# Kernel optimization log

Hardware: AMD Instinct MI355X
Metric: run time of the kernel (lower is better)

The kernel has to match this reference:

```python
import jax, jax.numpy as jnp
import numpy as np

EPS = 1e-5
NUM_MEM_TOKENS = 16
SEGMENT_SIZE = 512


def dpfp(x):
    # DPFP feature map (Schlag et al.), nu=1: doubles the last dim, all-nonnegative.
    x2 = jnp.concatenate([jax.nn.relu(x), jax.nn.relu(-x)], axis=-1)
    return x2 * jnp.roll(x2, 1, axis=-1)


def setup_inputs() -> dict:
    key = jax.random.key(0)
    ks = jax.random.split(key, 7)
    B, S, D, DM = 4, 4224, 1024, 64  # S = n_seg * (segment_size + num_mem_tokens) = 8*528
    scale = 0.02
    return {
        "hidden_states": jax.random.normal(ks[0], (B, S, D), jnp.float32),
        "model_output": jax.random.normal(ks[1], (B, S, D), jnp.float32),
        "W_mq": jax.random.normal(ks[2], (D, DM), jnp.float32) * scale,
        "W_mk": jax.random.normal(ks[3], (D, DM), jnp.float32) * scale,
        "W_mv": jax.random.normal(ks[4], (D, D), jnp.float32) * scale,
        "W_mb": jax.random.normal(ks[5], (D, D), jnp.float32) * scale,
        "b_mb": jnp.zeros((D,), jnp.float32),
    }


def reference(hidden_states, model_output, W_mq, W_mk, W_mv, W_mb, b_mb):
    B, S, D = hidden_states.shape
    L = SEGMENT_SIZE + NUM_MEM_TOKENS
    n_seg = S // L
    d_key = 2 * W_mq.shape[1]  # dpfp doubles feature dim

    # [n_seg, B, L, D]
    h = hidden_states.reshape(B, n_seg, L, D).transpose(1, 0, 2, 3)
    m = model_output.reshape(B, n_seg, L, D).transpose(1, 0, 2, 3)

    def step(carry, seg):
        W_mem, z = carry  # [B, d_key, D], [B, d_key]
        hid, mo = seg     # [B, L, D] each
        # --- associate: linear-attention read of compressive memory ---
        q = dpfp(hid @ W_mq)                                   # [B, L, d_key]
        num = jnp.einsum('blk,bkd->bld', q, W_mem)             # [B, L, D]
        den = jnp.einsum('blk,bk->bl', q, z)[..., None] + EPS
        assoc = num / den
        # --- delta-rule memory update from memory tokens of segment output ---
        mem = (assoc + mo)[:, -NUM_MEM_TOKENS:]                # [B, M, D]
        k = dpfp(mem @ W_mk)                                   # [B, M, d_key]
        v = mem @ W_mv                                         # [B, M, D]
        gate = jax.nn.sigmoid(mem @ W_mb + b_mb)               # [B, M, D]
        prev = jnp.einsum('bmk,bkd->bmd', k, W_mem) / (
            jnp.einsum('bmk,bk->bm', k, z)[..., None] + EPS)   # correction (old value)
        new_info = gate * (v - prev)
        W_mem = W_mem + jnp.einsum('bmk,bmd->bkd', k, new_info)
        z = z + k.sum(axis=1)
        return (W_mem, z), assoc

    W0 = jnp.zeros((B, d_key, D), hidden_states.dtype)
    z0 = jnp.zeros((B, d_key), hidden_states.dtype)
    _, assocs = jax.lax.scan(step, (W0, z0), (h, m))           # [n_seg, B, L, D]
    association = jnp.tanh(assocs.transpose(1, 0, 2, 3).reshape(B, S, D))
    return model_output + association
```

## Files before the change

kernel.cpp:

```cpp
#include <hip/hip_runtime.h>
#include <hip/hip_bf16.h>

#define EPS 1e-5f

typedef short s8v __attribute__((ext_vector_type(8)));
typedef short s4v __attribute__((ext_vector_type(4)));
typedef float f4v __attribute__((ext_vector_type(4)));

__device__ __forceinline__ unsigned short f2bf(float f) {
  unsigned u = __builtin_bit_cast(unsigned, f);
  u = u + 0x7FFFu + ((u >> 16) & 1u);
  return (unsigned short)(u >> 16);
}
__device__ __forceinline__ float bf2f(unsigned short h) {
  unsigned u = ((unsigned)h) << 16;
  return __builtin_bit_cast(float, u);
}
__device__ __forceinline__ float fast_tanh(float x) {
  float e = __expf(2.0f * x);
  return 1.0f - 2.0f / (e + 1.0f);
}
__device__ __forceinline__ float fast_sigmoid(float x) {
  return 1.0f / (1.0f + __expf(-x));
}

__global__ __launch_bounds__(256) void transpose_kernel(
    const float* __restrict__ W_mq, const float* __restrict__ W_mk,
    const float* __restrict__ W_mv, const float* __restrict__ W_mb,
    unsigned short* __restrict__ W_mqT, unsigned short* __restrict__ W_mkT,
    unsigned short* __restrict__ W_mvT, unsigned short* __restrict__ W_mbT) {
  __shared__ float tile[32][33];
  int bid = blockIdx.x;
  const float* src; unsigned short* dst; int N, t0;
  if (bid < 64)        { src = W_mq; dst = W_mqT; N = 64;   t0 = bid; }
  else if (bid < 128)  { src = W_mk; dst = W_mkT; N = 64;   t0 = bid - 64; }
  else if (bid < 1152) { src = W_mv; dst = W_mvT; N = 1024; t0 = bid - 128; }
  else                 { src = W_mb; dst = W_mbT; N = 1024; t0 = bid - 1152; }
  const int K = 1024;
  int tk = t0 & 31, tn = t0 >> 5;
  int k0 = tk * 32, n0 = tn * 32;
  int t = threadIdx.x;
  int cr = t >> 5, cc = t & 31;
#pragma unroll
  for (int u = 0; u < 4; u++) {
    int row = cr + u * 8;
    tile[row][cc] = src[(size_t)(k0 + row) * N + n0 + cc];
  }
  __syncthreads();
#pragma unroll
  for (int u = 0; u < 4; u++) {
    int nl = cr + u * 8;
    dst[(size_t)(n0 + nl) * K + k0 + cc] = f2bf(tile[cc][nl]);
  }
}

__global__ __launch_bounds__(128) void q_kernel(
    const float* __restrict__ HS, const unsigned short* __restrict__ W_mqT,
    unsigned short* __restrict__ Q) {
  __shared__ __align__(16) union { float y[16 * 64]; unsigned short kq[16 * 128]; } lds;
  int t = threadIdx.x, wv = t >> 6, lane = t & 63, m = lane & 15, q = lane >> 4;
  int r0 = blockIdx.x * 16;
  const float* ap = HS + (size_t)(r0 + m) * 1024 + wv * 512 + q * 8;
  const unsigned short* bp = W_mqT + (size_t)m * 1024 + wv * 512 + q * 8;
  f4v acc[4] = {f4v{0,0,0,0}, f4v{0,0,0,0}, f4v{0,0,0,0}, f4v{0,0,0,0}};
#pragma unroll 4
  for (int ks = 0; ks < 16; ks++) {
    int k0 = ks * 32;
    f4v h0 = *(const f4v*)(ap + k0);
    f4v h1 = *(const f4v*)(ap + k0 + 4);
    s8v a;
    a[0] = (short)f2bf(h0[0]); a[1] = (short)f2bf(h0[1]);
    a[2] = (short)f2bf(h0[2]); a[3] = (short)f2bf(h0[3]);
    a[4] = (short)f2bf(h1[0]); a[5] = (short)f2bf(h1[1]);
    a[6] = (short)f2bf(h1[2]); a[7] = (short)f2bf(h1[3]);
#pragma unroll
    for (int nf = 0; nf < 4; nf++) {
      s8v b = *(const s8v*)(bp + nf * 16384 + k0);
      acc[nf] = __builtin_amdgcn_mfma_f32_16x16x32_bf16(a, b, acc[nf], 0, 0, 0);
    }
  }
  if (wv == 1) {
#pragma unroll
    for (int nf = 0; nf < 4; nf++)
#pragma unroll
      for (int i = 0; i < 4; i++)
        lds.y[(nf * 4 + i) * 64 + lane] = acc[nf][i];
  }
  __syncthreads();
  if (wv == 0) {
#pragma unroll
    for (int nf = 0; nf < 4; nf++)
#pragma unroll
      for (int i = 0; i < 4; i++)
        acc[nf][i] += lds.y[(nf * 4 + i) * 64 + lane];
    int srcl = (lane & 48) | ((m + 15) & 15);
#pragma unroll
    for (int i = 0; i < 4; i++) {
      float yp[4];
#pragma unroll
      for (int nf = 0; nf < 4; nf++) yp[nf] = __shfl(acc[nf][i], srcl);
      int r = q * 4 + i;
#pragma unroll
      for (int nf = 0; nf < 4; nf++) {
        float yv = acc[nf][i];
        float py = (m != 0) ? yp[nf] : (nf > 0 ? yp[nf - 1] : yp[3]);
        bool wrap = (m == 0 && nf == 0);
        float x2lo = wrap ? fmaxf(-py, 0.f) : fmaxf(py, 0.f);
        float x2hi = wrap ? fmaxf(py, 0.f) : fmaxf(-py, 0.f);
        lds.kq[r * 128 + nf * 16 + m]      = f2bf(fmaxf(yv, 0.f) * x2lo);
        lds.kq[r * 128 + 64 + nf * 16 + m] = f2bf(fmaxf(-yv, 0.f) * x2hi);
      }
    }
  }
  __syncthreads();
  {
    int row = t >> 3, ch = t & 7;
    unsigned short* qp = Q + (size_t)(r0 + row) * 128 + ch * 16;
    *(s8v*)(qp)     = *(const s8v*)&lds.kq[row * 128 + ch * 16];
    *(s8v*)(qp + 8) = *(const s8v*)&lds.kq[row * 128 + ch * 16 + 8];
  }
}

__device__ __forceinline__ void assoc_tile(
    const unsigned short* __restrict__ Qb, const unsigned short* __restrict__ WmemT_s,
    const float* __restrict__ z_s, const float* __restrict__ MO,
    float* __restrict__ OUT, unsigned short* __restrict__ mem_bf,
    int seg, int rt, int ct, int b, bool write_mem) {
  int lane = threadIdx.x & 63, m = lane & 15, q = lane >> 4;
  size_t grow = (size_t)b * 4224 + seg * 528 + rt * 16;
  const unsigned short* qp = Qb + (grow + m) * 128;
  const float* zp = z_s + b * 128 + q * 8;
  s8v a[4];
  float dp = 0.f;
#pragma unroll
  for (int ks = 0; ks < 4; ks++) {
    a[ks] = *(const s8v*)(qp + ks * 32 + q * 8);
    f4v z0 = *(const f4v*)(zp + ks * 32);
    f4v z1 = *(const f4v*)(zp + ks * 32 + 4);
#pragma unroll
    for (int j = 0; j < 4; j++) dp += bf2f((unsigned short)a[ks][j]) * z0[j];
#pragma unroll
    for (int j = 0; j < 4; j++) dp += bf2f((unsigned short)a[ks][j + 4]) * z1[j];
  }
  dp += __shfl_xor(dp, 16);
  dp += __shfl_xor(dp, 32);
  dp += EPS;
  f4v acc[4] = {f4v{0,0,0,0}, f4v{0,0,0,0}, f4v{0,0,0,0}, f4v{0,0,0,0}};
  const unsigned short* wp = WmemT_s + ((size_t)b * 1024 + ct * 64 + m) * 128;
#pragma unroll
  for (int ks = 0; ks < 4; ks++) {
#pragma unroll
    for (int nf = 0; nf < 4; nf++) {
      s8v bv = *(const s8v*)(wp + nf * 2048 + ks * 32 + q * 8);
      acc[nf] = __builtin_amdgcn_mfma_f32_16x16x32_bf16(a[ks], bv, acc[nf], 0, 0, 0);
    }
  }
#pragma unroll
  for (int i = 0; i < 4; i++) {
    float den = __shfl(dp, q * 4 + i);
    int lrow = rt * 16 + q * 4 + i;
    size_t rbase = ((size_t)b * 4224 + seg * 528 + lrow) * 1024;
#pragma unroll
    for (int nf = 0; nf < 4; nf++) {
      int col = ct * 64 + nf * 16 + m;
      float assoc = acc[nf][i] / den;
      float mov = MO[rbase + col];
      OUT[rbase + col] = mov + fast_tanh(assoc);
      if (write_mem)
        mem_bf[(size_t)(b * 16 + (lrow - 512)) * 1024 + col] = f2bf(assoc + mov);
    }
  }
}

__global__ __launch_bounds__(64) void a_mem_kernel(
    const unsigned short* __restrict__ Qb, const unsigned short* __restrict__ WmemT_s,
    const float* __restrict__ z_s, const float* __restrict__ MO,
    float* __restrict__ OUT, unsigned short* __restrict__ mem_bf, int seg) {
  assoc_tile(Qb, WmemT_s, z_s, MO, OUT, mem_bf, seg, 32, blockIdx.x, blockIdx.y, true);
}

__global__ __launch_bounds__(64) void a_bulk_kernel(
    const unsigned short* __restrict__ Qb, const unsigned short* __restrict__ hist,
    const float* __restrict__ zh, const float* __restrict__ MO,
    float* __restrict__ OUT) {
  int seg = blockIdx.z >> 2, b = blockIdx.z & 3;
  assoc_tile(Qb, hist + (size_t)seg * 524288, zh + seg * 512, MO, OUT, nullptr,
             seg, blockIdx.x, blockIdx.y, b, false);
}

__global__ __launch_bounds__(256) void update_kernel(
    const unsigned short* __restrict__ mem_bf, const unsigned short* __restrict__ W_mkT,
    const unsigned short* __restrict__ W_mvT, const unsigned short* __restrict__ W_mbT,
    const float* __restrict__ z_s, const unsigned short* __restrict__ WmemT_s,
    const float* __restrict__ b_mb, float* __restrict__ W_mem,
    unsigned short* __restrict__ WmemT_next, float* __restrict__ z_next) {
  int ct = blockIdx.x, b = blockIdx.y;
  __shared__ float y_lds[16 * 64];
  __shared__ __align__(16) float k_f[16 * 128];
  __shared__ __align__(16) unsigned short k_bf[16 * 128];
  __shared__ float part[256];
  __shared__ float kden_l[16];
  __shared__ float ni_lds[16 * 65];
  int t = threadIdx.x, wv = t >> 6, lane = t & 63, m = lane & 15, q = lane >> 4;
  const unsigned short* ap = mem_bf + (size_t)(b * 16 + m) * 1024;
  {
    const unsigned short* bp = W_mkT + (size_t)(wv * 16 + m) * 1024;
    f4v acy = {0, 0, 0, 0};
    for (int ks = 0; ks < 32; ks++) {
      s8v av = *(const s8v*)(ap + ks * 32 + q * 8);
      s8v bv = *(const s8v*)(bp + ks * 32 + q * 8);
      acy = __builtin_amdgcn_mfma_f32_16x16x32_bf16(av, bv, acy, 0, 0, 0);
    }
#pragma unroll
    for (int i = 0; i < 4; i++) y_lds[(q * 4 + i) * 64 + wv * 16 + m] = acy[i];
  }
  __syncthreads();
  {
    int r = t >> 4, jg = t & 15;
    const float* yr = &y_lds[r * 64];
    const float* zz = z_s + b * 128;
    float pd = 0.f;
#pragma unroll
    for (int u = 0; u < 8; u++) {
      int jj = jg * 8 + u, jm = (jj + 127) & 127;
      float yj = (jj < 64) ? yr[jj] : -yr[jj - 64];
      float ym = (jm < 64) ? yr[jm] : -yr[jm - 64];
      float kv = fmaxf(yj, 0.f) * fmaxf(ym, 0.f);
      k_f[r * 128 + jj] = kv;
      k_bf[r * 128 + jj] = f2bf(kv);
      pd += kv * zz[jj];
    }
    part[t] = pd;
  }
  __syncthreads();
  if (t < 16) {
    float s = 0.f;
#pragma unroll
    for (int jg = 0; jg < 16; jg++) s += part[t * 16 + jg];
    kden_l[t] = s + EPS;
  }
  __syncthreads();
  int c = ct * 64 + wv * 16 + m;
  f4v accv = {0,0,0,0}, accg = {0,0,0,0}, accp = {0,0,0,0};
  {
    const unsigned short* bvp = W_mvT + (size_t)c * 1024;
    const unsigned short* bgp = W_mbT + (size_t)c * 1024;
    for (int ks = 0; ks < 32; ks++) {
      s8v av = *(const s8v*)(ap + ks * 32 + q * 8);
      s8v bv = *(const s8v*)(bvp + ks * 32 + q * 8);
      s8v bg = *(const s8v*)(bgp + ks * 32 + q * 8);
      accv = __builtin_amdgcn_mfma_f32_16x16x32_bf16(av, bv, accv, 0, 0, 0);
      accg = __builtin_amdgcn_mfma_f32_16x16x32_bf16(av, bg, accg, 0, 0, 0);
    }
    const unsigned short* bmp = WmemT_s + ((size_t)b * 1024 + c) * 128;
#pragma unroll
    for (int ks = 0; ks < 4; ks++) {
      s8v ak = *(const s8v*)&k_bf[m * 128 + ks * 32 + q * 8];
      s8v bm = *(const s8v*)(bmp + ks * 32 + q * 8);
      accp = __builtin_amdgcn_mfma_f32_16x16x32_bf16(ak, bm, accp, 0, 0, 0);
    }
  }
  float bmb = b_mb[c];
#pragma unroll
  for (int i = 0; i < 4; i++) {
    int r = q * 4 + i;
    float prev = accp[i] / kden_l[r];
    float g = fast_sigmoid(accg[i] + bmb);
    ni_lds[r * 65 + wv * 16 + m] = g * (accv[i] - prev);
  }
  __syncthreads();
  int cl = t & 63, kg = t >> 6, cc = ct * 64 + cl;
  float niv[16];
#pragma unroll
  for (int mm = 0; mm < 16; mm++) niv[mm] = ni_lds[mm * 65 + cl];
  float delta[32];
#pragma unroll
  for (int jj = 0; jj < 32; jj++) delta[jj] = 0.f;
#pragma unroll
  for (int mm = 0; mm < 16; mm++) {
    const float* kb = &k_f[mm * 128 + kg * 32];
    float nv = niv[mm];
#pragma unroll
    for (int ch = 0; ch < 8; ch++) {
      f4v kv4 = *(const f4v*)(kb + ch * 4);
#pragma unroll
      for (int jj = 0; jj < 4; jj++) delta[ch * 4 + jj] += kv4[jj] * nv;
    }
  }
  float* wmp = W_mem + (size_t)b * 131072 + cc;
  unsigned short* wtp = WmemT_next + ((size_t)b * 1024 + cc) * 128 + kg * 32;
#pragma unroll
  for (int c8 = 0; c8 < 4; c8++) {
    s8v pk;
#pragma unroll
    for (int u = 0; u < 8; u++) {
      int kk = kg * 32 + c8 * 8 + u;
      float nv = wmp[(size_t)kk * 1024] + delta[c8 * 8 + u];
      wmp[(size_t)kk * 1024] = nv;
      pk[u] = (short)f2bf(nv);
    }
    *(s8v*)(wtp + c8 * 8) = pk;
  }
  if (ct == 0 && t < 128) {
    float s = 0.f;
#pragma unroll
    for (int r = 0; r < 16; r++) s += k_f[r * 128 + t];
    z_next[b * 128 + t] = z_s[b * 128 + t] + s;
  }
}

extern "C" void kernel_launch(void* const* d_in, const int* in_sizes, int n_in,
                              void* d_out, int out_size, void* d_ws, size_t ws_size,
                              hipStream_t stream) {
  const float* HS  = (const float*)d_in[0];
  const float* MO  = (const float*)d_in[1];
  const float* W_mq = (const float*)d_in[2];
  const float* W_mk = (const float*)d_in[3];
  const float* W_mv = (const float*)d_in[4];
  const float* W_mb = (const float*)d_in[5];
  const float* b_mb = (const float*)d_in[6];
  float* OUT = (float*)d_out;

  char* wsb = (char*)d_ws;
  float*          W_mem  = (float*)(wsb + 0);
  unsigned short* hist   = (unsigned short*)(wsb + 2097152);
  float*          zh     = (float*)(wsb + 11534336);
  unsigned short* Qb     = (unsigned short*)(wsb + 11552768);
  unsigned short* W_mqT  = (unsigned short*)(wsb + 15878144);
  unsigned short* W_mkT  = (unsigned short*)(wsb + 16009216);
  unsigned short* W_mvT  = (unsigned short*)(wsb + 16140288);
  unsigned short* W_mbT  = (unsigned short*)(wsb + 18237440);
  unsigned short* mem_bf = (unsigned short*)(wsb + 20334592);

  (void)hipMemsetAsync(wsb, 0, 3145728, stream);
  (void)hipMemsetAsync(wsb + 11534336, 0, 2048, stream);
  transpose_kernel<<<2176, 256, 0, stream>>>(W_mq, W_mk, W_mv, W_mb,
                                             W_mqT, W_mkT, W_mvT, W_mbT);
  q_kernel<<<1056, 128, 0, stream>>>(HS, W_mqT, Qb);
  for (int s = 0; s < 8; s++) {
    const unsigned short* hs = hist + (size_t)s * 524288;
    unsigned short* hn = hist + (size_t)(s + 1) * 524288;
    const float* zs = zh + s * 512;
    float* zn = zh + (s + 1) * 512;
    a_mem_kernel<<<dim3(16, 4), 64, 0, stream>>>(Qb, hs, zs, MO, OUT, mem_bf, s);
    update_kernel<<<dim3(16, 4), 256, 0, stream>>>(mem_bf, W_mkT, W_mvT, W_mbT,
                                                   zs, hs, b_mb, W_mem, hn, zn);
  }
  a_bulk_kernel<<<dim3(32, 16, 32), 64, 0, stream>>>(Qb, hist, zh, MO, OUT);
}
```

Before: 491.2 us.

## Fuse segment scan into one persistent kernel with grid barriers and LDS-resident memory

Replaces the 16 per-segment launches (assoc-of-memory-tokens plus update) with a single persistent 64-block scan kernel. Each block keeps its W_mem slice in fp32 and bf16 in shared memory, and blocks synchronise between the associate and update phases through an atomic-counter grid barrier. The bulk association kernel is also reworked to 256-thread blocks that stage results in LDS and write coalesced float4 outputs. The aim is to remove launch overhead and global W_mem round-trips. The cost is reliance on spin barriers, which assume all 64 blocks are co-resident, and low parallelism during the scan.

```diff
diff --git a/kernel.cpp b/kernel.cpp
--- a/kernel.cpp
+++ b/kernel.cpp
@@ -2,6 +2,7 @@
 #include <hip/hip_bf16.h>
 
 #define EPS 1e-5f
+#define NBLK 64
 
 typedef short s8v __attribute__((ext_vector_type(8)));
 typedef short s4v __attribute__((ext_vector_type(4)));
@@ -23,6 +24,7 @@
 __device__ __forceinline__ float fast_sigmoid(float x) {
   return 1.0f / (1.0f + __expf(-x));
 }
+__device__ __forceinline__ float frcp(float x) { return __builtin_amdgcn_rcpf(x); }
 
 __global__ __launch_bounds__(256) void transpose_kernel(
     const float* __restrict__ W_mq, const float* __restrict__ W_mk,
@@ -121,191 +123,254 @@
   }
 }
 
-__device__ __forceinline__ void assoc_tile(
-    const unsigned short* __restrict__ Qb, const unsigned short* __restrict__ WmemT_s,
-    const float* __restrict__ z_s, const float* __restrict__ MO,
-    float* __restrict__ OUT, unsigned short* __restrict__ mem_bf,
-    int seg, int rt, int ct, int b, bool write_mem) {
-  int lane = threadIdx.x & 63, m = lane & 15, q = lane >> 4;
-  size_t grow = (size_t)b * 4224 + seg * 528 + rt * 16;
-  const unsigned short* qp = Qb + (grow + m) * 128;
-  const float* zp = z_s + b * 128 + q * 8;
-  s8v a[4];
-  float dp = 0.f;
-#pragma unroll
-  for (int ks = 0; ks < 4; ks++) {
-    a[ks] = *(const s8v*)(qp + ks * 32 + q * 8);
-    f4v z0 = *(const f4v*)(zp + ks * 32);
-    f4v z1 = *(const f4v*)(zp + ks * 32 + 4);
-#pragma unroll
-    for (int j = 0; j < 4; j++) dp += bf2f((unsigned short)a[ks][j]) * z0[j];
-#pragma unroll
-    for (int j = 0; j < 4; j++) dp += bf2f((unsigned short)a[ks][j + 4]) * z1[j];
-  }
-  dp += __shfl_xor(dp, 16);
-  dp += __shfl_xor(dp, 32);
-  dp += EPS;
-  f4v acc[4] = {f4v{0,0,0,0}, f4v{0,0,0,0}, f4v{0,0,0,0}, f4v{0,0,0,0}};
-  const unsigned short* wp = WmemT_s + ((size_t)b * 1024 + ct * 64 + m) * 128;
-#pragma unroll
-  for (int ks = 0; ks < 4; ks++) {
-#pragma unroll
-    for (int nf = 0; nf < 4; nf++) {
-      s8v bv = *(const s8v*)(wp + nf * 2048 + ks * 32 + q * 8);
-      acc[nf] = __builtin_amdgcn_mfma_f32_16x16x32_bf16(a[ks], bv, acc[nf], 0, 0, 0);
-    }
-  }
-#pragma unroll
-  for (int i = 0; i < 4; i++) {
-    float den = __shfl(dp, q * 4 + i);
-    int lrow = rt * 16 + q * 4 + i;
-    size_t rbase = ((size_t)b * 4224 + seg * 528 + lrow) * 1024;
-#pragma unroll
-    for (int nf = 0; nf < 4; nf++) {
-      int col = ct * 64 + nf * 16 + m;
-      float assoc = acc[nf][i] / den;
-      float mov = MO[rbase + col];
-      OUT[rbase + col] = mov + fast_tanh(assoc);
-      if (write_mem)
-        mem_bf[(size_t)(b * 16 + (lrow - 512)) * 1024 + col] = f2bf(assoc + mov);
-    }
-  }
-}
-
-__global__ __launch_bounds__(64) void a_mem_kernel(
-    const unsigned short* __restrict__ Qb, const unsigned short* __restrict__ WmemT_s,
-    const float* __restrict__ z_s, const float* __restrict__ MO,
-    float* __restrict__ OUT, unsigned short* __restrict__ mem_bf, int seg) {
-  assoc_tile(Qb, WmemT_s, z_s, MO, OUT, mem_bf, seg, 32, blockIdx.x, blockIdx.y, true);
-}
-
-__global__ __launch_bounds__(64) void a_bulk_kernel(
-    const unsigned short* __restrict__ Qb, const unsigned short* __restrict__ hist,
-    const float* __restrict__ zh, const float* __restrict__ MO,
-    float* __restrict__ OUT) {
-  int seg = blockIdx.z >> 2, b = blockIdx.z & 3;
-  assoc_tile(Qb, hist + (size_t)seg * 524288, zh + seg * 512, MO, OUT, nullptr,
-             seg, blockIdx.x, blockIdx.y, b, false);
-}
-
-__global__ __launch_bounds__(256) void update_kernel(
-    const unsigned short* __restrict__ mem_bf, const unsigned short* __restrict__ W_mkT,
+__global__ __launch_bounds__(256, 1) void scan_kernel(
+    const unsigned short* __restrict__ Qb, const unsigned short* __restrict__ W_mkT,
     const unsigned short* __restrict__ W_mvT, const unsigned short* __restrict__ W_mbT,
-    const float* __restrict__ z_s, const unsigned short* __restrict__ WmemT_s,
-    const float* __restrict__ b_mb, float* __restrict__ W_mem,
-    unsigned short* __restrict__ WmemT_next, float* __restrict__ z_next) {
-  int ct = blockIdx.x, b = blockIdx.y;
+    const float* __restrict__ b_mb, const float* __restrict__ MO,
+    float* __restrict__ OUT, unsigned short* __restrict__ hist,
+    float* __restrict__ zh, unsigned short* __restrict__ mem_bf, int* bar) {
+  __shared__ float Wf[128 * 64];
+  __shared__ __align__(16) unsigned short Wbf[64 * 132];
+  __shared__ __align__(16) unsigned short mem_l[16 * 1032];
   __shared__ float y_lds[16 * 64];
   __shared__ __align__(16) float k_f[16 * 128];
   __shared__ __align__(16) unsigned short k_bf[16 * 128];
   __shared__ float part[256];
   __shared__ float kden_l[16];
   __shared__ float ni_lds[16 * 65];
+  __shared__ float z_l[128];
+
   int t = threadIdx.x, wv = t >> 6, lane = t & 63, m = lane & 15, q = lane >> 4;
-  const unsigned short* ap = mem_bf + (size_t)(b * 16 + m) * 1024;
-  {
-    const unsigned short* bp = W_mkT + (size_t)(wv * 16 + m) * 1024;
-    f4v acy = {0, 0, 0, 0};
-    for (int ks = 0; ks < 32; ks++) {
-      s8v av = *(const s8v*)(ap + ks * 32 + q * 8);
-      s8v bv = *(const s8v*)(bp + ks * 32 + q * 8);
-      acy = __builtin_amdgcn_mfma_f32_16x16x32_bf16(av, bv, acy, 0, 0, 0);
-    }
-#pragma unroll
-    for (int i = 0; i < 4; i++) y_lds[(q * 4 + i) * 64 + wv * 16 + m] = acy[i];
+  int ct = blockIdx.x & 15, b = blockIdx.x >> 4;
+
+  for (int i = t; i < 128 * 64; i += 256) Wf[i] = 0.f;
+  for (int i = t; i < 64 * 132; i += 256) Wbf[i] = 0;
+  if (t < 128) z_l[t] = 0.f;
+  __syncthreads();
+
+  for (int s = 0; s < 8; s++) {
+    {
+      int col = t >> 2, koff = (t & 3) * 32;
+      const unsigned short* srcp = &Wbf[col * 132 + koff];
+      unsigned short* dstp = hist + (size_t)s * 524288 +
+                             ((size_t)b * 1024 + ct * 64 + col) * 128 + koff;
+#pragma unroll
+      for (int u = 0; u < 4; u++) *(s8v*)(dstp + u * 8) = *(const s8v*)(srcp + u * 8);
+      if (ct == 0 && t < 128) zh[s * 512 + b * 128 + t] = z_l[t];
+    }
+    {
+      size_t grow = (size_t)b * 4224 + s * 528 + 512;
+      const unsigned short* qp = Qb + (grow + m) * 128;
+      s8v a[4];
+      float dp = 0.f;
+#pragma unroll
+      for (int ks = 0; ks < 4; ks++) {
+        a[ks] = *(const s8v*)(qp + ks * 32 + q * 8);
+#pragma unroll
+        for (int j = 0; j < 8; j++)
+          dp += bf2f((unsigned short)a[ks][j]) * z_l[ks * 32 + q * 8 + j];
+      }
+      dp += __shfl_xor(dp, 16);
+      dp += __shfl_xor(dp, 32);
+      dp += EPS;
+      f4v acc = {0, 0, 0, 0};
+#pragma unroll
+      for (int ks = 0; ks < 4; ks++) {
+        s8v bv = *(const s8v*)&Wbf[(wv * 16 + m) * 132 + ks * 32 + q * 8];
+        acc = __builtin_amdgcn_mfma_f32_16x16x32_bf16(a[ks], bv, acc, 0, 0, 0);
+      }
+      unsigned short* mb = mem_bf + (s & 1) * 65536;
+#pragma unroll
+      for (int i = 0; i < 4; i++) {
+        float rden = frcp(__shfl(dp, q * 4 + i));
+        int col = ct * 64 + wv * 16 + m;
+        size_t rbase = (grow + q * 4 + i) * 1024;
+        float assoc = acc[i] * rden;
+        float mov = MO[rbase + col];
+        OUT[rbase + col] = mov + fast_tanh(assoc);
+        mb[(size_t)(b * 16 + q * 4 + i) * 1024 + col] = f2bf(assoc + mov);
+      }
+    }
+    __syncthreads();
+    if (t == 0) {
+      __threadfence();
+      atomicAdd(bar + s, 1);
+      while (atomicAdd(bar + s, 0) < NBLK) __builtin_amdgcn_s_sleep(2);
+      __threadfence();
+    }
+    __syncthreads();
+    {
+      const unsigned short* srcp = mem_bf + (s & 1) * 65536 + b * 16384;
+      int r = t >> 4, c0 = (t & 15) * 64;
+#pragma unroll
+      for (int u = 0; u < 8; u++)
+        *(s8v*)&mem_l[r * 1032 + c0 + u * 8] = *(const s8v*)(srcp + r * 1024 + c0 + u * 8);
+    }
+    __syncthreads();
+    {
+      const unsigned short* ap2 = &mem_l[m * 1032];
+      const unsigned short* bp = W_mkT + (size_t)(wv * 16 + m) * 1024;
+      f4v acy = {0, 0, 0, 0};
+      for (int ks = 0; ks < 32; ks++) {
+        s8v av = *(const s8v*)(ap2 + ks * 32 + q * 8);
+        s8v bv = *(const s8v*)(bp + ks * 32 + q * 8);
+        acy = __builtin_amdgcn_mfma_f32_16x16x32_bf16(av, bv, acy, 0, 0, 0);
+      }
+#pragma unroll
+      for (int i = 0; i < 4; i++) y_lds[(q * 4 + i) * 64 + wv * 16 + m] = acy[i];
+    }
+    __syncthreads();
+    {
+      int r = t >> 4, jg = t & 15;
+      const float* yr = &y_lds[r * 64];
+      float pd = 0.f;
+#pragma unroll
+      for (int u = 0; u < 8; u++) {
+        int jj = jg * 8 + u, jm = (jj + 127) & 127;
+        float yj = (jj < 64) ? yr[jj] : -yr[jj - 64];
+        float ym = (jm < 64) ? yr[jm] : -yr[jm - 64];
+        float kv = fmaxf(yj, 0.f) * fmaxf(ym, 0.f);
+        k_f[r * 128 + jj] = kv;
+        k_bf[r * 128 + jj] = f2bf(kv);
+        pd += kv * z_l[jj];
+      }
+      part[t] = pd;
+    }
+    __syncthreads();
+    if (t < 16) {
+      float ssum = 0.f;
+#pragma unroll
+      for (int jg = 0; jg < 16; jg++) ssum += part[t * 16 + jg];
+      kden_l[t] = ssum + EPS;
+    }
+    __syncthreads();
+    {
+      int c = ct * 64 + wv * 16 + m;
+      const unsigned short* ap2 = &mem_l[m * 1032];
+      const unsigned short* bvp = W_mvT + (size_t)c * 1024;
+      const unsigned short* bgp = W_mbT + (size_t)c * 1024;
+      f4v accv = {0,0,0,0}, accg = {0,0,0,0}, accp = {0,0,0,0};
+      for (int ks = 0; ks < 32; ks++) {
+        s8v av = *(const s8v*)(ap2 + ks * 32 + q * 8);
+        s8v bv = *(const s8v*)(bvp + ks * 32 + q * 8);
+        s8v bg = *(const s8v*)(bgp + ks * 32 + q * 8);
+        accv = __builtin_amdgcn_mfma_f32_16x16x32_bf16(av, bv, accv, 0, 0, 0);
+        accg = __builtin_amdgcn_mfma_f32_16x16x32_bf16(av, bg, accg, 0, 0, 0);
+      }
+#pragma unroll
+      for (int ks = 0; ks < 4; ks++) {
+        s8v ak = *(const s8v*)&k_bf[m * 128 + ks * 32 + q * 8];
+        s8v bm = *(const s8v*)&Wbf[(wv * 16 + m) * 132 + ks * 32 + q * 8];
+        accp = __builtin_amdgcn_mfma_f32_16x16x32_bf16(ak, bm, accp, 0, 0, 0);
+      }
+      float bmb = b_mb[c];
+#pragma unroll
+      for (int i = 0; i < 4; i++) {
+        int r = q * 4 + i;
+        float prev = accp[i] * frcp(kden_l[r]);
+        float g = fast_sigmoid(accg[i] + bmb);
+        ni_lds[r * 65 + wv * 16 + m] = g * (accv[i] - prev);
+      }
+    }
+    __syncthreads();
+    {
+      int cl = t & 63, kg = t >> 6;
+      float niv[16];
+#pragma unroll
+      for (int mm = 0; mm < 16; mm++) niv[mm] = ni_lds[mm * 65 + cl];
+      float delta[32];
+#pragma unroll
+      for (int jj = 0; jj < 32; jj++) delta[jj] = 0.f;
+#pragma unroll
+      for (int mm = 0; mm < 16; mm++) {
+        const float* kb = &k_f[mm * 128 + kg * 32];
+        float nv = niv[mm];
+#pragma unroll
+        for (int ch = 0; ch < 8; ch++) {
+          f4v kv4 = *(const f4v*)(kb + ch * 4);
+#pragma unroll
+          for (int jj = 0; jj < 4; jj++) delta[ch * 4 + jj] += kv4[jj] * nv;
+        }
+      }
+#pragma unroll
+      for (int c8 = 0; c8 < 4; c8++) {
+        s8v pk;
+#pragma unroll
+        for (int u = 0; u < 8; u++) {
+          int kk = kg * 32 + c8 * 8 + u;
+          float nv = Wf[kk * 64 + cl] + delta[c8 * 8 + u];
+          Wf[kk * 64 + cl] = nv;
+          pk[u] = (short)f2bf(nv);
+        }
+        *(s8v*)&Wbf[cl * 132 + kg * 32 + c8 * 8] = pk;
+      }
+      if (t < 128) {
+        float ssum = 0.f;
+#pragma unroll
+        for (int r = 0; r < 16; r++) ssum += k_f[r * 128 + t];
+        z_l[t] += ssum;
+      }
+    }
+    __syncthreads();
+  }
+}
+
+__global__ __launch_bounds__(256) void a_bulk_kernel(
+    const unsigned short* __restrict__ Qb, const unsigned short* __restrict__ hist,
+    const float* __restrict__ zh, const float* __restrict__ MO,
+    float* __restrict__ OUT) {
+  __shared__ float as_l[64 * 65];
+  int t = threadIdx.x, wv = t >> 6, lane = t & 63, m = lane & 15, q = lane >> 4;
+  int rt4 = blockIdx.x, ct = blockIdx.y;
+  int seg = blockIdx.z >> 2, b = blockIdx.z & 3;
+  const unsigned short* Wm = hist + (size_t)seg * 524288 + ((size_t)b * 1024 + ct * 64) * 128;
+  const float* zp = zh + seg * 512 + b * 128;
+  size_t grow = (size_t)b * 4224 + seg * 528 + rt4 * 64 + wv * 16;
+  const unsigned short* qp = Qb + (grow + m) * 128;
+  s8v a[4];
+  float dp = 0.f;
+#pragma unroll
+  for (int ks = 0; ks < 4; ks++) {
+    a[ks] = *(const s8v*)(qp + ks * 32 + q * 8);
+    f4v z0 = *(const f4v*)(zp + ks * 32 + q * 8);
+    f4v z1 = *(const f4v*)(zp + ks * 32 + q * 8 + 4);
+#pragma unroll
+    for (int j = 0; j < 4; j++) dp += bf2f((unsigned short)a[ks][j]) * z0[j];
+#pragma unroll
+    for (int j = 0; j < 4; j++) dp += bf2f((unsigned short)a[ks][j + 4]) * z1[j];
+  }
+  dp += __shfl_xor(dp, 16);
+  dp += __shfl_xor(dp, 32);
+  dp += EPS;
+  f4v acc[4] = {f4v{0,0,0,0}, f4v{0,0,0,0}, f4v{0,0,0,0}, f4v{0,0,0,0}};
+#pragma unroll
+  for (int ks = 0; ks < 4; ks++) {
+#pragma unroll
+    for (int nf = 0; nf < 4; nf++) {
+      s8v bv = *(const s8v*)(Wm + (size_t)(nf * 16 + m) * 128 + ks * 32 + q * 8);
+      acc[nf] = __builtin_amdgcn_mfma_f32_16x16x32_bf16(a[ks], bv, acc[nf], 0, 0, 0);
+    }
+  }
+#pragma unroll
+  for (int i = 0; i < 4; i++) {
+    float rden = frcp(__shfl(dp, q * 4 + i));
+#pragma unroll
+    for (int nf = 0; nf < 4; nf++)
+      as_l[(wv * 16 + q * 4 + i) * 65 + nf * 16 + m] = acc[nf][i] * rden;
   }
   __syncthreads();
   {
-    int r = t >> 4, jg = t & 15;
-    const float* yr = &y_lds[r * 64];
-    const float* zz = z_s + b * 128;
-    float pd = 0.f;
-#pragma unroll
-    for (int u = 0; u < 8; u++) {
-      int jj = jg * 8 + u, jm = (jj + 127) & 127;
-      float yj = (jj < 64) ? yr[jj] : -yr[jj - 64];
-      float ym = (jm < 64) ? yr[jm] : -yr[jm - 64];
-      float kv = fmaxf(yj, 0.f) * fmaxf(ym, 0.f);
-      k_f[r * 128 + jj] = kv;
-      k_bf[r * 128 + jj] = f2bf(kv);
-      pd += kv * zz[jj];
-    }
-    part[t] = pd;
-  }
-  __syncthreads();
-  if (t < 16) {
-    float s = 0.f;
-#pragma unroll
-    for (int jg = 0; jg < 16; jg++) s += part[t * 16 + jg];
-    kden_l[t] = s + EPS;
-  }
-  __syncthreads();
-  int c = ct * 64 + wv * 16 + m;
-  f4v accv = {0,0,0,0}, accg = {0,0,0,0}, accp = {0,0,0,0};
-  {
-    const unsigned short* bvp = W_mvT + (size_t)c * 1024;
-    const unsigned short* bgp = W_mbT + (size_t)c * 1024;
-    for (int ks = 0; ks < 32; ks++) {
-      s8v av = *(const s8v*)(ap + ks * 32 + q * 8);
-      s8v bv = *(const s8v*)(bvp + ks * 32 + q * 8);
-      s8v bg = *(const s8v*)(bgp + ks * 32 + q * 8);
-      accv = __builtin_amdgcn_mfma_f32_16x16x32_bf16(av, bv, accv, 0, 0, 0);
-      accg = __builtin_amdgcn_mfma_f32_16x16x32_bf16(av, bg, accg, 0, 0, 0);
-    }
-    const unsigned short* bmp = WmemT_s + ((size_t)b * 1024 + c) * 128;
-#pragma unroll
-    for (int ks = 0; ks < 4; ks++) {
-      s8v ak = *(const s8v*)&k_bf[m * 128 + ks * 32 + q * 8];
-      s8v bm = *(const s8v*)(bmp + ks * 32 + q * 8);
-      accp = __builtin_amdgcn_mfma_f32_16x16x32_bf16(ak, bm, accp, 0, 0, 0);
-    }
-  }
-  float bmb = b_mb[c];
-#pragma unroll
-  for (int i = 0; i < 4; i++) {
-    int r = q * 4 + i;
-    float prev = accp[i] / kden_l[r];
-    float g = fast_sigmoid(accg[i] + bmb);
-    ni_lds[r * 65 + wv * 16 + m] = g * (accv[i] - prev);
-  }
-  __syncthreads();
-  int cl = t & 63, kg = t >> 6, cc = ct * 64 + cl;
-  float niv[16];
-#pragma unroll
-  for (int mm = 0; mm < 16; mm++) niv[mm] = ni_lds[mm * 65 + cl];
-  float delta[32];
-#pragma unroll
-  for (int jj = 0; jj < 32; jj++) delta[jj] = 0.f;
-#pragma unroll
-  for (int mm = 0; mm < 16; mm++) {
-    const float* kb = &k_f[mm * 128 + kg * 32];
-    float nv = niv[mm];
-#pragma unroll
-    for (int ch = 0; ch < 8; ch++) {
-      f4v kv4 = *(const f4v*)(kb + ch * 4);
-#pragma unroll
-      for (int jj = 0; jj < 4; jj++) delta[ch * 4 + jj] += kv4[jj] * nv;
-    }
-  }
-  float* wmp = W_mem + (size_t)b * 131072 + cc;
-  unsigned short* wtp = WmemT_next + ((size_t)b * 1024 + cc) * 128 + kg * 32;
-#pragma unroll
-  for (int c8 = 0; c8 < 4; c8++) {
-    s8v pk;
-#pragma unroll
-    for (int u = 0; u < 8; u++) {
-      int kk = kg * 32 + c8 * 8 + u;
-      float nv = wmp[(size_t)kk * 1024] + delta[c8 * 8 + u];
-      wmp[(size_t)kk * 1024] = nv;
-      pk[u] = (short)f2bf(nv);
-    }
-    *(s8v*)(wtp + c8 * 8) = pk;
-  }
-  if (ct == 0 && t < 128) {
-    float s = 0.f;
-#pragma unroll
-    for (int r = 0; r < 16; r++) s += k_f[r * 128 + t];
-    z_next[b * 128 + t] = z_s[b * 128 + t] + s;
+    int r = t >> 2, cchunk = (t & 3) * 16;
+    size_t rbase = ((size_t)b * 4224 + seg * 528 + rt4 * 64 + r) * 1024 + ct * 64 + cchunk;
+    const float* ar = &as_l[r * 65 + cchunk];
+#pragma unroll
+    for (int u = 0; u < 4; u++) {
+      f4v mo = *(const f4v*)(MO + rbase + u * 4);
+      f4v o;
+#pragma unroll
+      for (int j = 0; j < 4; j++) o[j] = mo[j] + fast_tanh(ar[u * 4 + j]);
+      *(f4v*)(OUT + rbase + u * 4) = o;
+    }
   }
 }
 
@@ -322,29 +387,21 @@
   float* OUT = (float*)d_out;
 
   char* wsb = (char*)d_ws;
-  float*          W_mem  = (float*)(wsb + 0);
-  unsigned short* hist   = (unsigned short*)(wsb + 2097152);
-  float*          zh     = (float*)(wsb + 11534336);
-  unsigned short* Qb     = (unsigned short*)(wsb + 11552768);
-  unsigned short* W_mqT  = (unsigned short*)(wsb + 15878144);
-  unsigned short* W_mkT  = (unsigned short*)(wsb + 16009216);
-  unsigned short* W_mvT  = (unsigned short*)(wsb + 16140288);
-  unsigned short* W_mbT  = (unsigned short*)(wsb + 18237440);
-  unsigned short* mem_bf = (unsigned short*)(wsb + 20334592);
-
-  (void)hipMemsetAsync(wsb, 0, 3145728, stream);
-  (void)hipMemsetAsync(wsb + 11534336, 0, 2048, stream);
+  unsigned short* hist   = (unsigned short*)(wsb + 0);
+  float*          zh     = (float*)(wsb + 8388608);
+  unsigned short* Qb     = (unsigned short*)(wsb + 8404992);
+  unsigned short* W_mqT  = (unsigned short*)(wsb + 12730368);
+  unsigned short* W_mkT  = (unsigned short*)(wsb + 12861440);
+  unsigned short* W_mvT  = (unsigned short*)(wsb + 12992512);
+  unsigned short* W_mbT  = (unsigned short*)(wsb + 15089664);
+  unsigned short* mem_bf = (unsigned short*)(wsb + 17186816);
+  int*            bar    = (int*)(wsb + 17448960);
+
+  (void)hipMemsetAsync(bar, 0, 64, stream);
   transpose_kernel<<<2176, 256, 0, stream>>>(W_mq, W_mk, W_mv, W_mb,
                                              W_mqT, W_mkT, W_mvT, W_mbT);
   q_kernel<<<1056, 128, 0, stream>>>(HS, W_mqT, Qb);
-  for (int s = 0; s < 8; s++) {
-    const unsigned short* hs = hist + (size_t)s * 524288;
-    unsigned short* hn = hist + (size_t)(s + 1) * 524288;
-    const float* zs = zh + s * 512;
-    float* zn = zh + (s + 1) * 512;
-    a_mem_kernel<<<dim3(16, 4), 64, 0, stream>>>(Qb, hs, zs, MO, OUT, mem_bf, s);
-    update_kernel<<<dim3(16, 4), 256, 0, stream>>>(mem_bf, W_mkT, W_mvT, W_mbT,
-                                                   zs, hs, b_mb, W_mem, hn, zn);
-  }
-  a_bulk_kernel<<<dim3(32, 16, 32), 64, 0, stream>>>(Qb, hist, zh, MO, OUT);
-}
+  scan_kernel<<<NBLK, 256, 0, stream>>>(Qb, W_mkT, W_mvT, W_mbT, b_mb, MO, OUT,
+                                        hist, zh, mem_bf, bar);
+  a_bulk_kernel<<<dim3(8, 16, 32), 256, 0, stream>>>(Qb, hist, zh, MO, OUT);
+}
```

Result: faster. 467.1 us (-4.9%).
